# Kernel tuning notes

Hardware: AMD Instinct MI355X
Metric: run time of the kernel (lower is better)

Reference implementation:

```python
import jax, jax.numpy as jnp
import numpy as np

D_MODEL = 1024
N_HEAD = 16
HEAD_DIM = D_MODEL // N_HEAD
D_FF = int(D_MODEL * 4.0)
B, T = 2, 2048


def rms_norm(x, eps=1e-6):
    return x * jax.lax.rsqrt(jnp.mean(jnp.square(x), axis=-1, keepdims=True) + eps)


def rope_tables(T, head_dim):
    # half-truncated RoPE: first quarter of dims get real freqs, next quarter zeros
    angular_freq = (1.0 / 1024.0) ** jnp.linspace(0.0, 1.0, head_dim // 4, dtype=jnp.float32)
    angular_freq = jnp.concatenate([angular_freq, jnp.zeros(head_dim // 4, jnp.float32)])
    theta = jnp.arange(T, dtype=jnp.float32)[:, None] * angular_freq[None, :]  # [T, head_dim//2]
    return jnp.cos(theta), jnp.sin(theta)


def apply_rope(x, cos, sin):
    # x: [B, H, T, D]; cos/sin: [T, D//2]
    x1, x2 = jnp.split(x.astype(jnp.float32), 2, axis=-1)
    c = cos[None, None]
    s = sin[None, None]
    y1 = x1 * c + x2 * s
    y2 = -x1 * s + x2 * c
    return jnp.concatenate([y1, y2], axis=-1).astype(x.dtype)


def setup_inputs() -> dict:
    key = jax.random.key(0)
    ks = jax.random.split(key, 10)
    x = jax.random.normal(ks[0], (B, T, D_MODEL), jnp.float32)
    block_mask = jnp.tril(jnp.ones((T, T), jnp.bool_))  # causal
    sc = 1.0 / np.sqrt(D_MODEL)
    Wqkv = jax.random.normal(ks[1], (D_MODEL, 3 * D_MODEL), jnp.float32) * sc
    bqkv = jnp.zeros((3 * D_MODEL,), jnp.float32)
    Wo = jax.random.normal(ks[2], (D_MODEL, D_MODEL), jnp.float32) * sc
    bo = jnp.zeros((D_MODEL,), jnp.float32)
    W1 = jax.random.normal(ks[3], (D_MODEL, D_FF), jnp.float32) * sc
    b1 = jnp.zeros((D_FF,), jnp.float32)
    W2 = jax.random.normal(ks[4], (D_FF, D_MODEL), jnp.float32) * (1.0 / np.sqrt(D_FF))
    b2 = jnp.zeros((D_MODEL,), jnp.float32)
    return {"x": x, "block_mask": block_mask, "Wqkv": Wqkv, "bqkv": bqkv,
            "Wo": Wo, "bo": bo, "W1": W1, "b1": b1, "W2": W2, "b2": b2}


def reference(x, block_mask, Wqkv, bqkv, Wo, bo, W1, b1, W2, b2):
    Bq, Tq, D = x.shape
    cos, sin = rope_tables(Tq, HEAD_DIM)

    def attn(h):
        qkv = h @ Wqkv + bqkv  # [B, T, 3D]
        qkv = qkv.reshape(Bq, Tq, 3, N_HEAD, HEAD_DIM)
        qkv = jnp.transpose(qkv, (2, 0, 3, 1, 4))  # [3, B, H, T, d]
        q, k, v = qkv[0], qkv[1], qkv[2]
        q, k = rms_norm(q), rms_norm(k)
        q, k = apply_rope(q, cos, sin), apply_rope(k, cos, sin)
        scores = jnp.einsum('bhtd,bhsd->bhts', q, k) / np.sqrt(HEAD_DIM)
        scores = jnp.where(block_mask[None, None], scores, jnp.float32(-1e30))
        p = jax.nn.softmax(scores, axis=-1)
        o = jnp.einsum('bhts,bhsd->bhtd', p, v)
        o = jnp.transpose(o, (0, 2, 1, 3)).reshape(Bq, Tq, D)
        return o @ Wo + bo

    def mlp(h):
        return jax.nn.gelu(h @ W1 + b1) @ W2 + b2

    x = x + attn(rms_norm(x))
    x = x + mlp(rms_norm(x))
    return x
```

## Files before the change

### kernel.cpp

```cpp
#include <hip/hip_runtime.h>
#include <hip/hip_bf16.h>


typedef __attribute__((ext_vector_type(8))) short short8;
typedef __attribute__((ext_vector_type(4))) float f32x4;
typedef __attribute__((ext_vector_type(4))) unsigned short u16x4;
typedef __attribute__((ext_vector_type(8))) unsigned short u16x8;

#define MROWS 4096
#define DMODEL 1024
#define DFF 4096
#define NH 16
#define HD 64
#define SEQ 2048

static __device__ __forceinline__ unsigned short f2bf(float f) {
    union { __hip_bfloat16 b; unsigned short u; } cv;
    cv.b = __float2bfloat16(f);
    return cv.u;
}

static __device__ __forceinline__ void gload_lds16(const void* g, void* l) {
    __builtin_amdgcn_global_load_lds(
        (const __attribute__((address_space(1))) unsigned int*)g,
        (__attribute__((address_space(3))) unsigned int*)l, 16, 0, 0);
}

static __device__ __forceinline__ int xcd_swizzle(int id, int nwg) {
    const int nx = 8;
    const int q = nwg / nx, r = nwg % nx;
    const int xcd = id % nx, loc = id / nx;
    return (xcd < r ? xcd * (q + 1) : r * (q + 1) + (xcd - r) * q) + loc;
}

__global__ void cast_transpose(const float* __restrict__ W,
                               unsigned short* __restrict__ Wt, int K, int N) {
    __shared__ float tile[32][33];
    const int tx = threadIdx.x & 31;
    const int ty = threadIdx.x >> 5;
    const int n0 = blockIdx.x * 32, k0 = blockIdx.y * 32;
#pragma unroll
    for (int i = 0; i < 4; ++i) {
        int kk = ty + i * 8;
        tile[kk][tx] = W[(long)(k0 + kk) * N + n0 + tx];
    }
    __syncthreads();
#pragma unroll
    for (int i = 0; i < 4; ++i) {
        int nn = ty + i * 8;
        Wt[(long)(n0 + nn) * K + k0 + tx] = f2bf(tile[tx][nn]);
    }
}

__global__ void rope_table(float* __restrict__ cosT, float* __restrict__ sinT) {
    const int t = blockIdx.x, j = threadIdx.x;
    float th = (j < 16) ? (float)t * exp2f(-(10.0f / 15.0f) * (float)j) : 0.0f;
    cosT[t * 32 + j] = cosf(th);
    sinT[t * 32 + j] = sinf(th);
}

__global__ void rmsnorm_cast(const float* __restrict__ xin,
                             unsigned short* __restrict__ hout) {
    const int row = blockIdx.x;
    const float4 v = ((const float4*)(xin + (long)row * DMODEL))[threadIdx.x];
    float ss = v.x * v.x + v.y * v.y + v.z * v.z + v.w * v.w;
#pragma unroll
    for (int m = 32; m >= 1; m >>= 1) ss += __shfl_xor(ss, m);
    __shared__ float part[4];
    if ((threadIdx.x & 63) == 0) part[threadIdx.x >> 6] = ss;
    __syncthreads();
    const float tot = part[0] + part[1] + part[2] + part[3];
    const float sc = rsqrtf(tot * (1.0f / (float)DMODEL) + 1e-6f);
    ushort4 o;
    o.x = f2bf(v.x * sc); o.y = f2bf(v.y * sc);
    o.z = f2bf(v.z * sc); o.w = f2bf(v.w * sc);
    ((ushort4*)hout)[(long)row * (DMODEL / 4) + threadIdx.x] = o;
}

template <int EPI>
__launch_bounds__(512, 2)
__global__ void gemm256(const short* __restrict__ A, const short* __restrict__ Bt,
                        const float* __restrict__ bias,
                        float* __restrict__ outF, unsigned short* __restrict__ outB,
                        int N, int K) {
    __shared__ __align__(16) short As[4][128 * 64];
    __shared__ __align__(16) short Bs[4][128 * 64];
    const int tid = threadIdx.x;
    const int lane = tid & 63, w = tid >> 6;
    const int wr = w >> 2, wc = w & 3;
    const int l16 = lane & 15, lhi = lane >> 4;

    const int nwg = gridDim.x * gridDim.y;
    int id = xcd_swizzle(blockIdx.y * gridDim.x + blockIdx.x, nwg);
    const int bx = id % gridDim.x, by = id / gridDim.x;
    const long rowA0 = (long)by * 256;
    const long rowB0 = (long)bx * 256;

    const f32x4 fz = {0.f, 0.f, 0.f, 0.f};
    f32x4 acc[8][4];
#pragma unroll
    for (int m = 0; m < 8; ++m)
#pragma unroll
        for (int n = 0; n < 4; ++n) acc[m][n] = fz;

    auto stage = [&](int kt, int b) {
        const int k0 = kt << 5;
#pragma unroll
        for (int pass = 0; pass < 2; ++pass) {
            const int c = pass * 512 + tid;
            const int line = c >> 3, pch = c & 7;
            const int lch = pch ^ (line & 7);
            const int row = ((lch >> 2) << 7) + line;
            const int kc = (lch & 3) << 3;
            gload_lds16(A + (rowA0 + row) * K + k0 + kc, (char*)&As[b][0] + c * 16);
            gload_lds16(Bt + (rowB0 + row) * K + k0 + kc, (char*)&Bs[b][0] + c * 16);
        }
    };
    auto compute = [&](int b) {
        const short* Ab = &As[b][0];
        const short* Bb = &Bs[b][0];
        short8 af[8], bf[4];
#pragma unroll
        for (int m = 0; m < 8; ++m) {
            const int line = m * 16 + l16;
            const int pch = ((wr << 2) + lhi) ^ (line & 7);
            af[m] = *(const short8*)(Ab + line * 64 + pch * 8);
        }
#pragma unroll
        for (int n = 0; n < 4; ++n) {
            const int row = wc * 64 + n * 16 + l16;
            const int line = row & 127;
            const int pch = (((row >> 7) << 2) + lhi) ^ (line & 7);
            bf[n] = *(const short8*)(Bb + line * 64 + pch * 8);
        }
#pragma unroll
        for (int m = 0; m < 8; ++m)
#pragma unroll
            for (int n = 0; n < 4; ++n)
                acc[m][n] = __builtin_amdgcn_mfma_f32_16x16x32_bf16(
                    af[m], bf[n], acc[m][n], 0, 0, 0);
    };

    const int ktiles = K >> 5;
    stage(0, 0);
    stage(1, 1);
    stage(2, 2);
    for (int t = 0; t < ktiles; ++t) {
        const int rem = ktiles - 1 - t;
        if (rem >= 2)      asm volatile("s_waitcnt vmcnt(8)" ::: "memory");
        else if (rem == 1) asm volatile("s_waitcnt vmcnt(4)" ::: "memory");
        else               asm volatile("s_waitcnt vmcnt(0)" ::: "memory");
        __builtin_amdgcn_s_barrier();
        __builtin_amdgcn_sched_barrier(0);
        if (t + 3 < ktiles) stage(t + 3, (t + 3) & 3);
        compute(t & 3);
    }

#pragma unroll
    for (int m = 0; m < 8; ++m) {
        const long r0 = rowA0 + wr * 128 + m * 16 + lhi * 4;
#pragma unroll
        for (int n = 0; n < 4; ++n) {
            const long cc = rowB0 + wc * 64 + n * 16 + l16;
            const float bv = bias[cc];
#pragma unroll
            for (int j = 0; j < 4; ++j) {
                const long idx = (r0 + j) * N + cc;
                float v = acc[m][n][j] + bv;
                if (EPI == 2) {
                    float g = 0.5f * v *
                        (1.0f + tanhf(0.7978845608028654f * (v + 0.044715f * v * v * v)));
                    outB[idx] = f2bf(g);
                } else {
                    outF[idx] = v;
                }
            }
        }
    }
}

template <int EPI, int BN, int BK>
__launch_bounds__(256)
__global__ void gemm_bt(const short* __restrict__ A, const short* __restrict__ Bt,
                        const float* __restrict__ bias, const float* __restrict__ res,
                        float* __restrict__ outF, unsigned short* __restrict__ outB,
                        int N, int K) {
    constexpr int NF = BN / 32;
    constexpr int CPR = BK / 8;
    __shared__ short As[2][128 * BK];
    __shared__ short Bs[2][BN * BK];
    const int tid = threadIdx.x;
    const int lane = tid & 63, w = tid >> 6;
    const int wr = w >> 1, wc = w & 1;
    const int l16 = lane & 15, lhi = lane >> 4;

    const int nwg = gridDim.x * gridDim.y;
    int id = xcd_swizzle(blockIdx.y * gridDim.x + blockIdx.x, nwg);
    const int bx = id % gridDim.x, by = id / gridDim.x;
    const long rowA0 = (long)by * 128;
    const long rowB0 = (long)bx * BN;

    const f32x4 fz = {0.f, 0.f, 0.f, 0.f};
    f32x4 acc[4][NF];
#pragma unroll
    for (int m = 0; m < 4; ++m)
#pragma unroll
        for (int n = 0; n < NF; ++n) acc[m][n] = fz;

    auto stage = [&](int kt, int b) {
        const int k0 = kt * BK;
#pragma unroll
        for (int it = 0; it < BK / 16; ++it) {
            const int c = it * 256 + tid;
            const int r = c / CPR, col = (c % CPR) * 8;
            gload_lds16(A + (rowA0 + r) * K + k0 + col, (char*)As[b] + c * 16);
        }
#pragma unroll
        for (int it = 0; it < (BN * BK) / 2048; ++it) {
            const int c = it * 256 + tid;
            const int r = c / CPR, col = (c % CPR) * 8;
            gload_lds16(Bt + (rowB0 + r) * K + k0 + col, (char*)Bs[b] + c * 16);
        }
    };
    auto compute = [&](int b) {
#pragma unroll
        for (int kk = 0; kk < BK / 32; ++kk) {
            short8 af[4], bf[NF];
#pragma unroll
            for (int m = 0; m < 4; ++m)
                af[m] = *(const short8*)(&As[b][0] + (wr * 64 + m * 16 + l16) * BK + kk * 32 + lhi * 8);
#pragma unroll
            for (int n = 0; n < NF; ++n)
                bf[n] = *(const short8*)(&Bs[b][0] + (wc * (BN / 2) + n * 16 + l16) * BK + kk * 32 + lhi * 8);
#pragma unroll
            for (int m = 0; m < 4; ++m)
#pragma unroll
                for (int n = 0; n < NF; ++n)
                    acc[m][n] = __builtin_amdgcn_mfma_f32_16x16x32_bf16(
                        af[m], bf[n], acc[m][n], 0, 0, 0);
        }
    };

    const int ktiles = K / BK;
    stage(0, 0);
    __syncthreads();
    int cur = 0;
    for (int kt = 0; kt < ktiles; ++kt) {
        if (kt + 1 < ktiles) stage(kt + 1, cur ^ 1);
        compute(cur);
        __syncthreads();
        cur ^= 1;
    }

#pragma unroll
    for (int m = 0; m < 4; ++m) {
        const long r0 = rowA0 + wr * 64 + m * 16 + lhi * 4;
#pragma unroll
        for (int n = 0; n < NF; ++n) {
            const long cc = rowB0 + wc * (BN / 2) + n * 16 + l16;
            const float bv = bias[cc];
#pragma unroll
            for (int j = 0; j < 4; ++j) {
                const long idx = (r0 + j) * N + cc;
                float v = acc[m][n][j] + bv;
                if (EPI == 1) v += res[idx];
                if (EPI == 2) {
                    float g = 0.5f * v *
                        (1.0f + tanhf(0.7978845608028654f * (v + 0.044715f * v * v * v)));
                    outB[idx] = f2bf(g);
                } else {
                    outF[idx] = v;
                }
            }
        }
    }
}

__global__ void qkv_post(const float* __restrict__ qkv, const float* __restrict__ cosT,
                         const float* __restrict__ sinT, unsigned short* __restrict__ Qo,
                         unsigned short* __restrict__ Ko) {
    const int lane = threadIdx.x & 63;
    const int g = blockIdx.x * 4 + (threadIdx.x >> 6);
    const int row = g >> 4, h = g & 15;
    const int b = row >> 11, t = row & 2047;
    const float* base = qkv + (long)row * 3072 + h * 64;
    float q = base[lane];
    float k = base[1024 + lane];
    float sq = q * q, sk = k * k;
#pragma unroll
    for (int m = 32; m >= 1; m >>= 1) {
        sq += __shfl_xor(sq, m);
        sk += __shfl_xor(sk, m);
    }
    q *= rsqrtf(sq * (1.0f / 64.0f) + 1e-6f);
    k *= rsqrtf(sk * (1.0f / 64.0f) + 1e-6f);
    const int j = lane & 31;
    const float c = cosT[t * 32 + j], s = sinT[t * 32 + j];
    const float q2 = __shfl_xor(q, 32), k2 = __shfl_xor(k, 32);
    const float sgn = (lane < 32) ? 1.0f : -1.0f;
    const float qr = q * c + sgn * q2 * s;
    const float kr = k * c + sgn * k2 * s;
    const long o = ((long)(b * 16 + h) * SEQ + t) * 64 + lane;
    Qo[o] = f2bf(qr * 0.125f);
    Ko[o] = f2bf(kr);
}

__global__ void transpose_v(const float* __restrict__ qkv,
                            unsigned short* __restrict__ Vt) {
    __shared__ float tile[64][65];
    const int tid = threadIdx.x;
    const int bh = blockIdx.x, tt = blockIdx.y;
    const int b = bh >> 4, h = bh & 15;
    const int tr = tid >> 2, c0 = (tid & 3) * 16;
    const float* src = qkv + ((long)(b * SEQ + tt * 64 + tr)) * 3072 + 2048 + h * 64 + c0;
#pragma unroll
    for (int i = 0; i < 4; ++i) {
        float4 v = ((const float4*)src)[i];
        tile[tr][c0 + i * 4 + 0] = v.x;
        tile[tr][c0 + i * 4 + 1] = v.y;
        tile[tr][c0 + i * 4 + 2] = v.z;
        tile[tr][c0 + i * 4 + 3] = v.w;
    }
    __syncthreads();
    const int d = tid >> 2, t0 = (tid & 3) * 16;
    unsigned short* dst = Vt + ((long)bh * 64 + d) * SEQ + tt * 64 + t0;
#pragma unroll
    for (int half = 0; half < 2; ++half) {
        u16x8 o;
#pragma unroll
        for (int e = 0; e < 8; ++e) o[e] = f2bf(tile[t0 + half * 8 + e][d]);
        *(u16x8*)(dst + half * 8) = o;
    }
}

__launch_bounds__(256)
__global__ void attn_fwd(const short* __restrict__ Qg, const short* __restrict__ Kg,
                         const short* __restrict__ Vtg, unsigned short* __restrict__ Og) {
    __shared__ short Ks[2][64 * 64];
    __shared__ short Vs[2][64 * 64];
    __shared__ char Ps[4][2048];
    const int tid = threadIdx.x, lane = tid & 63, w = tid >> 6;
    const int l16 = lane & 15, lhi = lane >> 4;
    const int id = xcd_swizzle(blockIdx.y * gridDim.x + blockIdx.x, 512);
    const int bh = id >> 4;
    const int ip = id & 15;
    const int bb = bh >> 4, hh = bh & 15;
    const long base_q = (long)bh * (SEQ * 64);
    char* Pw = &Ps[w][0];
    const int swz = (l16 & 7) << 4;
    const f32x4 fz = {0.f, 0.f, 0.f, 0.f};

#pragma unroll 1
    for (int rep = 0; rep < 2; ++rep) {
        const int qt = rep ? ip : 31 - ip;
        short8 aq0, aq1;
        {
            const short* Qp = Qg + base_q + (long)(qt * 64 + w * 16) * 64;
            aq0 = *(const short8*)(Qp + l16 * 64 + lhi * 8);
            aq1 = *(const short8*)(Qp + l16 * 64 + 32 + lhi * 8);
        }
        float mrow = -1e30f, lrow = 0.f;
        f32x4 oacc[4];
#pragma unroll
        for (int n = 0; n < 4; ++n) oacc[n] = fz;

        auto stage = [&](int kt, int b) {
            const short* Kp = Kg + base_q + (long)kt * 64 * 64;
            const short* Vp = Vtg + base_q + (long)kt * 64;
#pragma unroll
            for (int it = 0; it < 2; ++it) {
                const int c = it * 256 + tid;
                const int r = c >> 3;
                const int col = ((c & 7) ^ (r & 7)) << 3;
                gload_lds16(Kp + r * 64 + col, (char*)&Ks[b][0] + c * 16);
                gload_lds16(Vp + (long)r * SEQ + col, (char*)&Vs[b][0] + c * 16);
            }
        };

        stage(0, 0);
        __syncthreads();
        int cur = 0;
        for (int kt = 0; kt <= qt; ++kt) {
            if (kt < qt) stage(kt + 1, cur ^ 1);
            const short* KsC = &Ks[cur][0];
            const short* VsC = &Vs[cur][0];

            f32x4 s[4];
            __builtin_amdgcn_s_setprio(1);
#pragma unroll
            for (int n = 0; n < 4; ++n) {
                const int kr = n * 16 + l16;
                short8 bk0 = *(const short8*)(KsC + kr * 64 + ((lhi ^ (kr & 7)) << 3));
                short8 bk1 = *(const short8*)(KsC + kr * 64 + (((lhi + 4) ^ (kr & 7)) << 3));
                f32x4 z = fz;
                z = __builtin_amdgcn_mfma_f32_16x16x32_bf16(bk0, aq0, z, 0, 0, 0);
                s[n] = __builtin_amdgcn_mfma_f32_16x16x32_bf16(bk1, aq1, z, 0, 0, 0);
            }
            __builtin_amdgcn_s_setprio(0);
            if (kt == qt) {
#pragma unroll
                for (int n = 0; n < 4; ++n)
#pragma unroll
                    for (int j = 0; j < 4; ++j)
                        if (n * 16 + lhi * 4 + j > w * 16 + l16) s[n][j] = -1e30f;
            }

            float pm = s[0][0];
#pragma unroll
            for (int n = 0; n < 4; ++n)
#pragma unroll
                for (int j = 0; j < 4; ++j) pm = fmaxf(pm, s[n][j]);
            pm = fmaxf(pm, __shfl_xor(pm, 16));
            pm = fmaxf(pm, __shfl_xor(pm, 32));
            if (!__all(pm <= mrow + 8.f)) {
                const float newm = fmaxf(mrow, pm);
                const float sc = __expf(mrow - newm);
                mrow = newm;
                lrow *= sc;
#pragma unroll
                for (int j = 0; j < 4; ++j) {
                    const float scj = __shfl(sc, lhi * 4 + j);
#pragma unroll
                    for (int n = 0; n < 4; ++n) oacc[n][j] *= scj;
                }
            }
            float ps = 0.f;
#pragma unroll
            for (int n = 0; n < 4; ++n)
#pragma unroll
                for (int j = 0; j < 4; ++j) {
                    const float p = __expf(s[n][j] - mrow);
                    s[n][j] = p;
                    ps += p;
                }
            ps += __shfl_xor(ps, 16);
            ps += __shfl_xor(ps, 32);
            lrow += ps;

#pragma unroll
            for (int n = 0; n < 4; ++n) {
                u16x4 pk;
                pk[0] = f2bf(s[n][0]);
                pk[1] = f2bf(s[n][1]);
                pk[2] = f2bf(s[n][2]);
                pk[3] = f2bf(s[n][3]);
                *(u16x4*)(Pw + ((l16 * 128 + n * 32 + lhi * 8) ^ swz)) = pk;
            }

            __builtin_amdgcn_s_setprio(1);
#pragma unroll
            for (int ks = 0; ks < 2; ++ks) {
                short8 pa = *(const short8*)(Pw + ((l16 * 128 + ks * 64 + lhi * 16) ^ swz));
#pragma unroll
                for (int n = 0; n < 4; ++n) {
                    const int dr = n * 16 + l16;
                    short8 vb = *(const short8*)(VsC + dr * 64 + ((((ks << 2) + lhi) ^ (dr & 7)) << 3));
                    oacc[n] = __builtin_amdgcn_mfma_f32_16x16x32_bf16(pa, vb, oacc[n], 0, 0, 0);
                }
            }
            __builtin_amdgcn_s_setprio(0);
            __syncthreads();
            cur ^= 1;
        }

#pragma unroll
        for (int j = 0; j < 4; ++j) {
            const float lr = __shfl(lrow, lhi * 4 + j);
            const int qrow = qt * 64 + w * 16 + lhi * 4 + j;
            const long orow = (long)bb * SEQ + qrow;
#pragma unroll
            for (int n = 0; n < 4; ++n)
                Og[orow * DMODEL + hh * 64 + n * 16 + l16] = f2bf(oacc[n][j] / lr);
        }
    }
}

extern "C" void kernel_launch(void* const* d_in, const int* in_sizes, int n_in,
                              void* d_out, int out_size, void* d_ws, size_t ws_size,
                              hipStream_t stream) {
    const float* x    = (const float*)d_in[0];
    const float* Wqkv = (const float*)d_in[2];
    const float* bqkv = (const float*)d_in[3];
    const float* Wo   = (const float*)d_in[4];
    const float* bo   = (const float*)d_in[5];
    const float* W1   = (const float*)d_in[6];
    const float* b1   = (const float*)d_in[7];
    const float* W2   = (const float*)d_in[8];
    const float* b2   = (const float*)d_in[9];
    float* out = (float*)d_out;

    char* ws = (char*)d_ws;
    auto alloc = [&](size_t b) {
        char* p = ws;
        ws += (b + 255) & ~(size_t)255;
        return p;
    };
    short* WqkvT = (short*)alloc(3072ull * 1024 * 2);
    short* WoT   = (short*)alloc(1024ull * 1024 * 2);
    short* W1T   = (short*)alloc(4096ull * 1024 * 2);
    short* W2T   = (short*)alloc(1024ull * 4096 * 2);
    float* cosT  = (float*)alloc(2048ull * 32 * 4);
    float* sinT  = (float*)alloc(2048ull * 32 * 4);
    short* hbuf  = (short*)alloc((size_t)MROWS * DMODEL * 2);
    short* Qb    = (short*)alloc(32ull * SEQ * 64 * 2);
    short* Kb    = (short*)alloc(32ull * SEQ * 64 * 2);
    short* Vtb   = (short*)alloc(32ull * 64 * SEQ * 2);
    short* Ob    = (short*)alloc((size_t)MROWS * DMODEL * 2);
    float* x1    = (float*)alloc((size_t)MROWS * DMODEL * 4);
    char*  big   = alloc((size_t)MROWS * 3072 * 4);
    float* qkv   = (float*)big;
    unsigned short* act = (unsigned short*)big;

    cast_transpose<<<dim3(96, 32), 256, 0, stream>>>(Wqkv, (unsigned short*)WqkvT, 1024, 3072);
    cast_transpose<<<dim3(32, 32), 256, 0, stream>>>(Wo, (unsigned short*)WoT, 1024, 1024);
    cast_transpose<<<dim3(128, 32), 256, 0, stream>>>(W1, (unsigned short*)W1T, 1024, 4096);
    cast_transpose<<<dim3(32, 128), 256, 0, stream>>>(W2, (unsigned short*)W2T, 4096, 1024);
    rope_table<<<2048, 32, 0, stream>>>(cosT, sinT);
    rmsnorm_cast<<<MROWS, 256, 0, stream>>>(x, (unsigned short*)hbuf);
    gemm256<0><<<dim3(12, 16), 512, 0, stream>>>(hbuf, WqkvT, bqkv, qkv, nullptr, 3072, 1024);
    qkv_post<<<16384, 256, 0, stream>>>(qkv, cosT, sinT,
                                        (unsigned short*)Qb, (unsigned short*)Kb);
    transpose_v<<<dim3(32, 32), 256, 0, stream>>>(qkv, (unsigned short*)Vtb);
    attn_fwd<<<dim3(16, 32), 256, 0, stream>>>(Qb, Kb, Vtb, (unsigned short*)Ob);
    gemm_bt<1, 64, 64><<<dim3(16, 32), 256, 0, stream>>>(Ob, WoT, bo, x, x1, nullptr, 1024, 1024);
    rmsnorm_cast<<<MROWS, 256, 0, stream>>>(x1, (unsigned short*)hbuf);
    gemm256<2><<<dim3(16, 16), 512, 0, stream>>>(hbuf, W1T, b1, nullptr, act, 4096, 1024);
    gemm_bt<1, 64, 64><<<dim3(16, 32), 256, 0, stream>>>((const short*)act, W2T, b2, x1, out, nullptr, 1024, 4096);
}
```

Measured before the change: 419.0 us.

## Triple-buffer residual GEMM with XOR-swizzled LDS and single barrier per k-tile

Replaces the templated double-buffered gemm_bt used for the output projection and the second MLP GEMM with a specialized 128x64x64 kernel. It adds a three-stage LDS ring with explicit vmcnt waits and one barrier per k-tile, an XOR swizzle of 16-byte chunks to avoid LDS bank conflicts on the fragment reads, and a hint of two blocks per CU. The goal is to hide global-load latency better and cut the per-iteration sync and LDS conflict cost. In exchange it uses more LDS per block and relies on hand-tuned waitcnt counts.

Result: faster. 392.9 us (-6.2%).

```diff
diff --git a/kernel.cpp b/kernel.cpp
--- a/kernel.cpp
+++ b/kernel.cpp
@@ -179,16 +179,12 @@
     }
 }
 
-template <int EPI, int BN, int BK>
-__launch_bounds__(256)
-__global__ void gemm_bt(const short* __restrict__ A, const short* __restrict__ Bt,
-                        const float* __restrict__ bias, const float* __restrict__ res,
-                        float* __restrict__ outF, unsigned short* __restrict__ outB,
-                        int N, int K) {
-    constexpr int NF = BN / 32;
-    constexpr int CPR = BK / 8;
-    __shared__ short As[2][128 * BK];
-    __shared__ short Bs[2][BN * BK];
+__launch_bounds__(256, 2)
+__global__ void gemm_rb64(const short* __restrict__ A, const short* __restrict__ Bt,
+                          const float* __restrict__ bias, const float* __restrict__ res,
+                          float* __restrict__ outF, int N, int K) {
+    __shared__ __align__(16) short As[3][128 * 64];
+    __shared__ __align__(16) short Bs[3][64 * 64];
     const int tid = threadIdx.x;
     const int lane = tid & 63, w = tid >> 6;
     const int wr = w >> 1, wc = w & 1;
@@ -198,79 +194,82 @@
     int id = xcd_swizzle(blockIdx.y * gridDim.x + blockIdx.x, nwg);
     const int bx = id % gridDim.x, by = id / gridDim.x;
     const long rowA0 = (long)by * 128;
-    const long rowB0 = (long)bx * BN;
+    const long rowB0 = (long)bx * 64;
 
     const f32x4 fz = {0.f, 0.f, 0.f, 0.f};
-    f32x4 acc[4][NF];
+    f32x4 acc[4][2];
 #pragma unroll
     for (int m = 0; m < 4; ++m)
 #pragma unroll
-        for (int n = 0; n < NF; ++n) acc[m][n] = fz;
+        for (int n = 0; n < 2; ++n) acc[m][n] = fz;
 
     auto stage = [&](int kt, int b) {
-        const int k0 = kt * BK;
-#pragma unroll
-        for (int it = 0; it < BK / 16; ++it) {
+        const int k0 = kt << 6;
+#pragma unroll
+        for (int it = 0; it < 4; ++it) {
             const int c = it * 256 + tid;
-            const int r = c / CPR, col = (c % CPR) * 8;
-            gload_lds16(A + (rowA0 + r) * K + k0 + col, (char*)As[b] + c * 16);
-        }
-#pragma unroll
-        for (int it = 0; it < (BN * BK) / 2048; ++it) {
+            const int row = c >> 3;
+            const int col = ((c & 7) ^ (row & 7)) << 3;
+            gload_lds16(A + (rowA0 + row) * K + k0 + col, (char*)&As[b][0] + c * 16);
+        }
+#pragma unroll
+        for (int it = 0; it < 2; ++it) {
             const int c = it * 256 + tid;
-            const int r = c / CPR, col = (c % CPR) * 8;
-            gload_lds16(Bt + (rowB0 + r) * K + k0 + col, (char*)Bs[b] + c * 16);
+            const int row = c >> 3;
+            const int col = ((c & 7) ^ (row & 7)) << 3;
+            gload_lds16(Bt + (rowB0 + row) * K + k0 + col, (char*)&Bs[b][0] + c * 16);
         }
     };
     auto compute = [&](int b) {
-#pragma unroll
-        for (int kk = 0; kk < BK / 32; ++kk) {
-            short8 af[4], bf[NF];
+        const short* Ab = &As[b][0];
+        const short* Bb = &Bs[b][0];
+#pragma unroll
+        for (int kk = 0; kk < 2; ++kk) {
+            short8 af[4], bf[2];
+#pragma unroll
+            for (int m = 0; m < 4; ++m) {
+                const int row = wr * 64 + m * 16 + l16;
+                const int pch = (kk * 4 + lhi) ^ (row & 7);
+                af[m] = *(const short8*)(Ab + row * 64 + pch * 8);
+            }
+#pragma unroll
+            for (int n = 0; n < 2; ++n) {
+                const int row = wc * 32 + n * 16 + l16;
+                const int pch = (kk * 4 + lhi) ^ (row & 7);
+                bf[n] = *(const short8*)(Bb + row * 64 + pch * 8);
+            }
 #pragma unroll
             for (int m = 0; m < 4; ++m)
-                af[m] = *(const short8*)(&As[b][0] + (wr * 64 + m * 16 + l16) * BK + kk * 32 + lhi * 8);
-#pragma unroll
-            for (int n = 0; n < NF; ++n)
-                bf[n] = *(const short8*)(&Bs[b][0] + (wc * (BN / 2) + n * 16 + l16) * BK + kk * 32 + lhi * 8);
-#pragma unroll
-            for (int m = 0; m < 4; ++m)
-#pragma unroll
-                for (int n = 0; n < NF; ++n)
+#pragma unroll
+                for (int n = 0; n < 2; ++n)
                     acc[m][n] = __builtin_amdgcn_mfma_f32_16x16x32_bf16(
                         af[m], bf[n], acc[m][n], 0, 0, 0);
         }
     };
 
-    const int ktiles = K / BK;
+    const int ktiles = K >> 6;
     stage(0, 0);
-    __syncthreads();
-    int cur = 0;
-    for (int kt = 0; kt < ktiles; ++kt) {
-        if (kt + 1 < ktiles) stage(kt + 1, cur ^ 1);
-        compute(cur);
-        __syncthreads();
-        cur ^= 1;
+    stage(1, 1);
+    for (int t = 0; t < ktiles; ++t) {
+        if (t + 1 < ktiles) asm volatile("s_waitcnt vmcnt(6)" ::: "memory");
+        else                asm volatile("s_waitcnt vmcnt(0)" ::: "memory");
+        __builtin_amdgcn_s_barrier();
+        __builtin_amdgcn_sched_barrier(0);
+        if (t + 2 < ktiles) stage(t + 2, (t + 2) % 3);
+        compute(t % 3);
     }
 
 #pragma unroll
     for (int m = 0; m < 4; ++m) {
         const long r0 = rowA0 + wr * 64 + m * 16 + lhi * 4;
 #pragma unroll
-        for (int n = 0; n < NF; ++n) {
-            const long cc = rowB0 + wc * (BN / 2) + n * 16 + l16;
+        for (int n = 0; n < 2; ++n) {
+            const long cc = rowB0 + wc * 32 + n * 16 + l16;
             const float bv = bias[cc];
 #pragma unroll
             for (int j = 0; j < 4; ++j) {
                 const long idx = (r0 + j) * N + cc;
-                float v = acc[m][n][j] + bv;
-                if (EPI == 1) v += res[idx];
-                if (EPI == 2) {
-                    float g = 0.5f * v *
-                        (1.0f + tanhf(0.7978845608028654f * (v + 0.044715f * v * v * v)));
-                    outB[idx] = f2bf(g);
-                } else {
-                    outF[idx] = v;
-                }
+                outF[idx] = acc[m][n][j] + bv + res[idx];
             }
         }
     }
@@ -522,8 +521,8 @@
                                         (unsigned short*)Qb, (unsigned short*)Kb);
     transpose_v<<<dim3(32, 32), 256, 0, stream>>>(qkv, (unsigned short*)Vtb);
     attn_fwd<<<dim3(16, 32), 256, 0, stream>>>(Qb, Kb, Vtb, (unsigned short*)Ob);
-    gemm_bt<1, 64, 64><<<dim3(16, 32), 256, 0, stream>>>(Ob, WoT, bo, x, x1, nullptr, 1024, 1024);
+    gemm_rb64<<<dim3(16, 32), 256, 0, stream>>>(Ob, WoT, bo, x, x1, 1024, 1024);
     rmsnorm_cast<<<MROWS, 256, 0, stream>>>(x1, (unsigned short*)hbuf);
     gemm256<2><<<dim3(16, 16), 512, 0, stream>>>(hbuf, W1T, b1, nullptr, act, 4096, 1024);
-    gemm_bt<1, 64, 64><<<dim3(16, 32), 256, 0, stream>>>((const short*)act, W2T, b2, x1, out, nullptr, 1024, 4096);
-}
+    gemm_rb64<<<dim3(16, 32), 256, 0, stream>>>((const short*)act, W2T, b2, x1, out, 1024, 4096);
+}
```
